# Performance work log

Measured on AMD Instinct MI355X. Metric: run time of the kernel, lower is better.

The kernel has to match this reference:

```python
import jax, jax.numpy as jnp
import numpy as np

B, T, C, H = 2, 2048, 2048, 16
HD = C // H  # 128
WINDOW = 2048


def setup_inputs() -> dict:
    key = jax.random.key(0)
    k0, k1, k2 = jax.random.split(key, 3)
    s = 0.02  # GPT-2 style init scale
    return {
        "x": jax.random.normal(k0, (B, T, C), jnp.float32),
        "w_attn": jax.random.normal(k1, (3 * C, C), jnp.float32) * s,
        "b_attn": jnp.zeros((3 * C,), jnp.float32),
        "w_proj": jax.random.normal(k2, (C, C), jnp.float32) * s,
        "b_proj": jnp.zeros((C,), jnp.float32),
    }


def reference(x, w_attn, b_attn, w_proj, b_proj):
    Bb, Tt, Cc = x.shape
    # fused qkv projection (torch Linear: y = x @ W^T + b)
    qkv = x @ w_attn.T + b_attn                       # [B, T, 3C]
    q, k, v = jnp.split(qkv, 3, axis=2)

    def to_heads(t):
        return t.reshape(Bb, Tt, H, HD).transpose(0, 2, 1, 3)  # [B, H, T, HD]

    q, k, v = to_heads(q), to_heads(k), to_heads(v)
    K = k.shape[2]  # kv length (== T, no past_kv)

    attn = jnp.einsum('bhqd,bhkd->bhqk', q, k) / jnp.sqrt(jnp.float32(HD))
    # Faithful to source: mask[:, :, T-1:T, :K] — single tril row T-1 broadcast
    # over all query positions (for prefill K==T this row is all ones).
    mask_row = jnp.arange(K) <= (Tt - 1)              # [K] bool
    attn = jnp.where(mask_row[None, None, None, :], attn, -jnp.inf)
    weights = jax.nn.softmax(attn, axis=-1)            # [B, H, T, K]
    # dropout p=0.0 (eval): identity
    ctx = jnp.einsum('bhqk,bhkd->bhqd', weights, v)    # [B, H, T, HD]
    ctx = ctx.transpose(0, 2, 1, 3).reshape(Bb, Tt, Cc)
    out = ctx @ w_proj.T + b_proj                      # [B, T, C]
    return (out, k, v)  # (context, present_kv)
```

## Files before the change

### kernel.cpp

```cpp
#include <hip/hip_runtime.h>
#include <hip/hip_bf16.h>
#include <cstdint>
#include <cstddef>
#include <cmath>

typedef __attribute__((ext_vector_type(8))) short short8;
typedef __attribute__((ext_vector_type(4))) short bf16x4;
typedef __attribute__((ext_vector_type(4))) float f32x4;

static constexpr int BB = 2, T = 2048, C = 2048, H = 16, HD = 128;
static constexpr int M = BB * T;
static constexpr size_t BTC = (size_t)BB * T * C;

__device__ __forceinline__ short f2bf(float f) {
    union { float f; uint32_t u; } v; v.f = f;
    uint32_t u = v.u;
    uint32_t r = (u + 0x7fffu + ((u >> 16) & 1u)) >> 16;
    return (short)r;
}

__device__ __forceinline__ short f2bf_fast(float f) {
    __hip_bfloat16 h = __float2bfloat16(f);
    return *reinterpret_cast<short*>(&h);
}

__device__ __forceinline__ void gl_lds16(const void* g, void* l) {
    __builtin_amdgcn_global_load_lds(
        (const __attribute__((address_space(1))) unsigned int*)g,
        (__attribute__((address_space(3))) unsigned int*)l, 16, 0, 0);
}

__global__ void cvt_bf16(const float* __restrict__ in, short* __restrict__ out, int n) {
    int i = (blockIdx.x * 256 + threadIdx.x) * 8;
    if (i >= n) return;
    float4 a = *(const float4*)(in + i);
    float4 b = *(const float4*)(in + i + 4);
    short8 o;
    o[0] = f2bf(a.x); o[1] = f2bf(a.y); o[2] = f2bf(a.z); o[3] = f2bf(a.w);
    o[4] = f2bf(b.x); o[5] = f2bf(b.y); o[6] = f2bf(b.z); o[7] = f2bf(b.w);
    *(short8*)(out + i) = o;
}

template<int NI, int EPI, int NBX>
__launch_bounds__(512, 2)
__global__ void gemm8p(const short* __restrict__ A, const short* __restrict__ Bw,
                       const float* __restrict__ bias, float* __restrict__ outF,
                       short* __restrict__ q_ws, short* __restrict__ k_ws, int Ndim) {
    extern __shared__ char lds[];
    constexpr int K = 2048, NKT = K / 64;
    constexpr int NCH = 4 + NI;
    constexpr int BUFSZ = 32768 + NI * 8192;

    int bid = blockIdx.x;
    int nwg = gridDim.x;
    int swz = (bid & 7) * (nwg >> 3) + (bid >> 3);
    int by = swz / NBX, bx = swz % NBX;
    int row0 = by * 256, col0 = bx * (NI * 64);

    int t = threadIdx.x, w = t >> 6, l = t & 63;
    int lr = l & 15, lg = l >> 4;
    int wr = w >> 2, wc = w & 3;

    const char* srcb[NCH];
    int dstoff[NCH];
#pragma unroll
    for (int c = 0; c < NCH; c++) {
        bool isA = c < 4;
        int coff = (isA ? c : c - 4) * 8192 + t * 16;
        int row = coff >> 7;
        int colb = (coff & 127) ^ ((row & 7) << 4);
        srcb[c] = isA ? (const char*)A + (size_t)(row0 + row) * (K * 2) + colb
                      : (const char*)Bw + (size_t)(col0 + row) * (K * 2) + colb;
        dstoff[c] = (isA ? 0 : 32768) + coff;
    }

    f32x4 acc[8][NI] = {};

#pragma unroll
    for (int c = 0; c < NCH; c++) gl_lds16(srcb[c], lds + dstoff[c]);
#pragma unroll
    for (int c = 0; c < NCH; c++) gl_lds16(srcb[c] + 128, lds + BUFSZ + dstoff[c]);
    asm volatile("s_waitcnt vmcnt(%0)" :: "n"(NCH) : "memory");
    __builtin_amdgcn_s_barrier();

    for (int kt = 0; kt < NKT; kt++) {
        char* base = lds + (kt & 1) * BUFSZ;
        const char* Bbase = base + 32768;
        int koff = (kt + 2) * 128;
        bool pf = (kt + 2 < NKT);

        short8 bfr[NI][2];
#pragma unroll
        for (int p = 0; p < 4; p++) {
            short8 af[2][2];
#pragma unroll
            for (int mi2 = 0; mi2 < 2; mi2++) {
                int row = wr * 128 + p * 32 + mi2 * 16 + lr;
#pragma unroll
                for (int ks = 0; ks < 2; ks++)
                    af[mi2][ks] = *(const short8*)(base + row * 128 +
                                  ((ks * 64 + lg * 16) ^ ((row & 7) << 4)));
            }
            if (p == 0) {
#pragma unroll
                for (int ni = 0; ni < NI; ni++) {
                    int row = wc * (NI * 16) + ni * 16 + lr;
#pragma unroll
                    for (int ks = 0; ks < 2; ks++)
                        bfr[ni][ks] = *(const short8*)(Bbase + row * 128 +
                                      ((ks * 64 + lg * 16) ^ ((row & 7) << 4)));
                }
            }
            __builtin_amdgcn_s_barrier();
            __builtin_amdgcn_s_setprio(1);
#pragma unroll
            for (int ks = 0; ks < 2; ks++)
#pragma unroll
                for (int mi2 = 0; mi2 < 2; mi2++)
#pragma unroll
                    for (int ni = 0; ni < NI; ni++)
                        acc[p * 2 + mi2][ni] = __builtin_amdgcn_mfma_f32_16x16x32_bf16(
                            af[mi2][ks], bfr[ni][ks], acc[p * 2 + mi2][ni], 0, 0, 0);
            __builtin_amdgcn_s_setprio(0);
            __builtin_amdgcn_sched_barrier(0);
            __builtin_amdgcn_s_barrier();

            if (p == 0 && pf) {
                asm volatile("" ::: "memory");
#pragma unroll
                for (int c = 4; c < NCH; c++) gl_lds16(srcb[c] + koff, base + dstoff[c]);
            }
            if (p == 1 && pf) {
                asm volatile("" ::: "memory");
                gl_lds16(srcb[0] + koff, base + dstoff[0]);
                gl_lds16(srcb[2] + koff, base + dstoff[2]);
            }
            if (p == 3) {
                if (pf) {
                    asm volatile("" ::: "memory");
                    gl_lds16(srcb[1] + koff, base + dstoff[1]);
                    gl_lds16(srcb[3] + koff, base + dstoff[3]);
                    asm volatile("s_waitcnt vmcnt(%0)" :: "n"(NCH) : "memory");
                } else {
                    asm volatile("s_waitcnt vmcnt(0)" ::: "memory");
                }
                __builtin_amdgcn_s_barrier();
            }
        }
    }

#pragma unroll
    for (int mi = 0; mi < 8; mi++) {
        int gr0 = row0 + wr * 128 + mi * 16 + lg * 4;
#pragma unroll
        for (int ni = 0; ni < NI; ni++) {
            int gc = col0 + wc * (NI * 16) + ni * 16 + lr;
            float bv = bias[gc];
            if (EPI == 0) {
                int sec = gc >> 11, cc = gc & 2047;
                int h = cc >> 7, d = cc & 127;
#pragma unroll
                for (int r = 0; r < 4; r++) {
                    float val = acc[mi][ni][r] + bv;
                    int gr = gr0 + r;
                    int b = gr >> 11, tt = gr & 2047;
                    size_t idx = ((size_t)(b * H + h) * T + tt) * HD + d;
                    if (sec == 0) {
                        q_ws[idx] = f2bf(val);
                    } else if (sec == 1) {
                        outF[BTC + idx] = val;
                        k_ws[idx] = f2bf(val);
                    } else {
                        outF[2 * BTC + idx] = val;
                    }
                }
            } else {
#pragma unroll
                for (int r = 0; r < 4; r++)
                    outF[(size_t)(gr0 + r) * Ndim + gc] = acc[mi][ni][r] + bv;
            }
        }
    }
}

__global__ void vtrans(const float* __restrict__ vin, short* __restrict__ vT) {
    __shared__ float tile[64 * 65];
    int blk = blockIdx.x;
    int bh = blk >> 6, rem = blk & 63;
    int t0 = (rem >> 1) * 64, d0 = (rem & 1) * 64;
    const float* src = vin + (size_t)bh * T * HD;
    short* dst = vT + (size_t)bh * HD * T;
    int t = threadIdx.x;
#pragma unroll
    for (int i = 0; i < 16; i++) {
        int idx = i * 256 + t;
        int r = idx >> 6, c = idx & 63;
        tile[r * 65 + c] = src[(size_t)(t0 + r) * HD + d0 + c];
    }
    __syncthreads();
#pragma unroll
    for (int i = 0; i < 16; i++) {
        int idx = i * 256 + t;
        int rd = idx >> 6, cc = idx & 63;
        dst[(size_t)(d0 + rd) * T + t0 + cc] = f2bf(tile[cc * 65 + rd]);
    }
}

__launch_bounds__(256, 2)
__global__ void attn_fwd(const short* __restrict__ q_ws, const short* __restrict__ k_ws,
                         const short* __restrict__ vT_ws, short* __restrict__ ctx) {
    __shared__ __attribute__((aligned(16))) char K_lds[2][64 * 256];
    __shared__ __attribute__((aligned(16))) char VT_lds[2][128 * 128];
    __shared__ __attribute__((aligned(16))) char P_lds[4][16 * 128];

    int bid = blockIdx.x;
    int blk = (bid & 7) * 64 + (bid >> 3);
    int bh = blk >> 4;
    int q0 = (blk & 15) * 128;
    int b = bh >> 4, h = bh & 15;
    int t = threadIdx.x, w = t >> 6, l = t & 63;
    int lr = l & 15, lg = l >> 4;
    int sw = (lr & 7) << 4;

    short8 qf[2][4];
#pragma unroll
    for (int qt = 0; qt < 2; qt++) {
        const short* Qp = q_ws + ((size_t)bh * T + q0 + w * 32 + qt * 16 + lr) * HD;
#pragma unroll
        for (int c = 0; c < 4; c++) qf[qt][c] = *(const short8*)(Qp + c * 32 + lg * 8);
    }

    const char* Kp = (const char*)(k_ws + (size_t)bh * T * HD);
    const short* VTp = vT_ws + (size_t)bh * HD * T;
    char* Pc = P_lds[w];

    const float SC = 0.12753123813884803f;
    float m[2] = {-INFINITY, -INFINITY}, lsum[2] = {0.f, 0.f};
    f32x4 acc[2][8] = {};

    auto STAGE = [&](int kt, int bsel) {
#pragma unroll
        for (int i = 0; i < 4; i++) {
            int off = i * 4096 + t * 16;
            int swzK = off ^ (((off >> 8) & 7) << 4);
            gl_lds16(Kp + (size_t)kt * 16384 + swzK, K_lds[bsel] + off);
            int swzV = off ^ (((off >> 7) & 7) << 4);
            int row = swzV >> 7, cole = (swzV & 127) >> 1;
            gl_lds16(VTp + (size_t)row * T + kt * 64 + cole, VT_lds[bsel] + off);
        }
    };

    STAGE(0, 0);
    asm volatile("s_waitcnt vmcnt(0)" ::: "memory");
    __syncthreads();

    for (int kt = 0; kt < T / 64; kt++) {
        int cur = kt & 1;
        if (kt + 1 < T / 64) STAGE(kt + 1, cur ^ 1);
        const char* Kc = K_lds[cur];
        const char* Vc = VT_lds[cur];

        f32x4 sacc[2][4] = {};
#pragma unroll
        for (int kj = 0; kj < 4; kj++) {
            int rowb = (kj * 16 + lr) * 256;
#pragma unroll
            for (int c = 0; c < 4; c++) {
                short8 kf = *(const short8*)(Kc + ((rowb + c * 64 + lg * 16) ^ sw));
                sacc[0][kj] = __builtin_amdgcn_mfma_f32_16x16x32_bf16(kf, qf[0][c], sacc[0][kj], 0, 0, 0);
                sacc[1][kj] = __builtin_amdgcn_mfma_f32_16x16x32_bf16(kf, qf[1][c], sacc[1][kj], 0, 0, 0);
            }
        }

#pragma unroll
        for (int qt = 0; qt < 2; qt++) {
            float t0 = fmaxf(fmaxf(sacc[qt][0][0], sacc[qt][0][1]), fmaxf(sacc[qt][0][2], sacc[qt][0][3]));
            float t1 = fmaxf(fmaxf(sacc[qt][1][0], sacc[qt][1][1]), fmaxf(sacc[qt][1][2], sacc[qt][1][3]));
            float t2 = fmaxf(fmaxf(sacc[qt][2][0], sacc[qt][2][1]), fmaxf(sacc[qt][2][2], sacc[qt][2][3]));
            float t3 = fmaxf(fmaxf(sacc[qt][3][0], sacc[qt][3][1]), fmaxf(sacc[qt][3][2], sacc[qt][3][3]));
            float xm = fmaxf(fmaxf(t0, t1), fmaxf(t2, t3)) * SC;
            xm = fmaxf(xm, __shfl_xor(xm, 16));
            xm = fmaxf(xm, __shfl_xor(xm, 32));

            if (!__all(xm <= m[qt] + 8.0f)) {
                float mn = fmaxf(m[qt], xm);
                float al = __builtin_exp2f(m[qt] - mn);
                m[qt] = mn;
                lsum[qt] *= al;
                float ar[4];
#pragma unroll
                for (int r = 0; r < 4; r++) ar[r] = __shfl(al, lg * 4 + r);
#pragma unroll
                for (int nj = 0; nj < 8; nj++)
#pragma unroll
                    for (int r = 0; r < 4; r++) acc[qt][nj][r] *= ar[r];
            }

            float s0 = 0.f;
#pragma unroll
            for (int kj = 0; kj < 4; kj++) {
                bf16x4 pk;
#pragma unroll
                for (int r = 0; r < 4; r++) {
                    float pv = __builtin_exp2f(__builtin_fmaf(sacc[qt][kj][r], SC, -m[qt]));
                    s0 += pv;
                    pk[r] = f2bf_fast(pv);
                }
                *(bf16x4*)(Pc + ((lr * 128 + kj * 32 + lg * 8) ^ sw)) = pk;
            }
            s0 += __shfl_xor(s0, 16);
            s0 += __shfl_xor(s0, 32);
            lsum[qt] += s0;

            asm volatile("s_waitcnt lgkmcnt(0)" ::: "memory");

#pragma unroll
            for (int c2 = 0; c2 < 2; c2++) {
                short8 pf = *(const short8*)(Pc + ((lr * 128 + c2 * 64 + lg * 16) ^ sw));
#pragma unroll
                for (int nj = 0; nj < 8; nj++) {
                    short8 vf = *(const short8*)(Vc + (((nj * 16 + lr) * 128 + c2 * 64 + lg * 16) ^ sw));
                    acc[qt][nj] = __builtin_amdgcn_mfma_f32_16x16x32_bf16(pf, vf, acc[qt][nj], 0, 0, 0);
                }
            }
        }

        asm volatile("s_waitcnt vmcnt(0)" ::: "memory");
        __syncthreads();
    }

#pragma unroll
    for (int qt = 0; qt < 2; qt++)
#pragma unroll
        for (int r = 0; r < 4; r++) {
            float rs = __shfl(lsum[qt], lg * 4 + r);
            float inv = 1.0f / rs;
            int tq = q0 + w * 32 + qt * 16 + lg * 4 + r;
            size_t base = ((size_t)b * T + tq) * C + h * HD;
#pragma unroll
            for (int nj = 0; nj < 8; nj++)
                ctx[base + nj * 16 + lr] = f2bf_fast(acc[qt][nj][r] * inv);
        }
}

extern "C" void kernel_launch(void* const* d_in, const int* in_sizes, int n_in,
                              void* d_out, int out_size, void* d_ws, size_t ws_size,
                              hipStream_t stream) {
    const float* x      = (const float*)d_in[0];
    const float* w_attn = (const float*)d_in[1];
    const float* b_attn = (const float*)d_in[2];
    const float* w_proj = (const float*)d_in[3];
    const float* b_proj = (const float*)d_in[4];
    float* out = (float*)d_out;

    char* ws = (char*)d_ws;
    short* x_bf  = (short*)ws;
    short* wp_bf = (short*)ws;
    short* wa_bf = (short*)(ws + 16777216);
    short* ctx   = (short*)(ws + 16777216);
    short* vT    = (short*)(ws + 41943040);

    short* q_ws = (short*)d_out;
    short* k_ws = (short*)d_out + BTC;

    hipFuncSetAttribute((const void*)gemm8p<3, 0, 32>,
                        hipFuncAttributeMaxDynamicSharedMemorySize, 114688);
    hipFuncSetAttribute((const void*)gemm8p<2, 1, 16>,
                        hipFuncAttributeMaxDynamicSharedMemorySize, 98304);

    cvt_bf16<<<4096, 256, 0, stream>>>(x, x_bf, (int)BTC);
    cvt_bf16<<<6144, 256, 0, stream>>>(w_attn, wa_bf, 3 * C * C);

    gemm8p<3, 0, 32><<<512, 512, 114688, stream>>>(x_bf, wa_bf, b_attn, out, q_ws, k_ws, 6144);

    vtrans<<<2048, 256, 0, stream>>>(out + 2 * BTC, vT);
    cvt_bf16<<<2048, 256, 0, stream>>>(w_proj, wp_bf, C * C);

    attn_fwd<<<512, 256, 0, stream>>>(q_ws, k_ws, vT, ctx);

    gemm8p<2, 1, 16><<<256, 512, 98304, stream>>>(ctx, wp_bf, b_proj, out, nullptr, nullptr, 2048);
}
```

Before: 293.7 us.

## Replace QKV GEMM with smaller-tile kernel and fuse V transpose into epilogue

```diff
diff --git a/kernel.cpp b/kernel.cpp
--- a/kernel.cpp
+++ b/kernel.cpp
@@ -41,11 +41,122 @@
     *(short8*)(out + i) = o;
 }
 
+__launch_bounds__(512, 4)
+__global__ void gemm_qkv128(const short* __restrict__ A, const short* __restrict__ Bw,
+                            const float* __restrict__ bias, float* __restrict__ outF,
+                            short* __restrict__ q_ws, short* __restrict__ k_ws,
+                            short* __restrict__ vT) {
+    extern __shared__ char lds[];
+    constexpr int K = 2048, NKT = K / 64;
+    constexpr int BUFSZ = 40960;
+
+    int bid = blockIdx.x;
+    int swz = (bid & 7) * 128 + (bid >> 3);
+    int by = swz >> 5, bx = swz & 31;
+    int row0 = by * 128, col0 = bx * 192;
+
+    int t = threadIdx.x, w = t >> 6, l = t & 63;
+    int lr = l & 15, lg = l >> 4;
+    int wr = w >> 2, wc = w & 3;
+
+    const char* srcb[5];
+    int dstoff[5];
+#pragma unroll
+    for (int c = 0; c < 5; c++) {
+        bool isA = c < 2;
+        int coff = (isA ? c : c - 2) * 8192 + t * 16;
+        int row = coff >> 7;
+        int colb = (coff & 127) ^ ((row & 7) << 4);
+        srcb[c] = isA ? (const char*)A + (size_t)(row0 + row) * (K * 2) + colb
+                      : (const char*)Bw + (size_t)(col0 + row) * (K * 2) + colb;
+        dstoff[c] = (isA ? 0 : 16384) + coff;
+    }
+
+    f32x4 acc[4][3] = {};
+
+#pragma unroll
+    for (int c = 0; c < 5; c++) gl_lds16(srcb[c], lds + dstoff[c]);
+#pragma unroll
+    for (int c = 0; c < 5; c++) gl_lds16(srcb[c] + 128, lds + BUFSZ + dstoff[c]);
+    asm volatile("s_waitcnt vmcnt(5)" ::: "memory");
+    __builtin_amdgcn_s_barrier();
+
+    for (int kt = 0; kt < NKT; kt++) {
+        char* base = lds + (kt & 1) * BUFSZ;
+        const char* Bbase = base + 16384;
+
+        short8 bfr[3][2];
+#pragma unroll
+        for (int ni = 0; ni < 3; ni++) {
+            int row = wc * 48 + ni * 16 + lr;
+            int rsw = (row & 7) << 4;
+#pragma unroll
+            for (int ks = 0; ks < 2; ks++)
+                bfr[ni][ks] = *(const short8*)(Bbase + row * 128 + ((ks * 64 + lg * 16) ^ rsw));
+        }
+        __builtin_amdgcn_s_setprio(1);
+#pragma unroll
+        for (int mi = 0; mi < 4; mi++) {
+            int row = wr * 64 + mi * 16 + lr;
+            int rsw = (row & 7) << 4;
+            const char* rp = base + row * 128;
+            short8 a0 = *(const short8*)(rp + ((lg * 16) ^ rsw));
+            short8 a1 = *(const short8*)(rp + ((64 + lg * 16) ^ rsw));
+#pragma unroll
+            for (int ni = 0; ni < 3; ni++) {
+                acc[mi][ni] = __builtin_amdgcn_mfma_f32_16x16x32_bf16(a0, bfr[ni][0], acc[mi][ni], 0, 0, 0);
+                acc[mi][ni] = __builtin_amdgcn_mfma_f32_16x16x32_bf16(a1, bfr[ni][1], acc[mi][ni], 0, 0, 0);
+            }
+        }
+        __builtin_amdgcn_s_setprio(0);
+
+        __builtin_amdgcn_s_barrier();
+        if (kt + 2 < NKT) {
+            int koff = (kt + 2) * 128;
+#pragma unroll
+            for (int c = 0; c < 5; c++) gl_lds16(srcb[c] + koff, base + dstoff[c]);
+            asm volatile("s_waitcnt vmcnt(5)" ::: "memory");
+        } else {
+            asm volatile("s_waitcnt vmcnt(0)" ::: "memory");
+        }
+        __builtin_amdgcn_s_barrier();
+    }
+
+#pragma unroll
+    for (int mi = 0; mi < 4; mi++) {
+        int gr0 = row0 + wr * 64 + mi * 16 + lg * 4;
+#pragma unroll
+        for (int ni = 0; ni < 3; ni++) {
+            int gc = col0 + wc * 48 + ni * 16 + lr;
+            float bv = bias[gc];
+            int sec = gc >> 11, cc = gc & 2047;
+            int h = cc >> 7, d = cc & 127;
+#pragma unroll
+            for (int r = 0; r < 4; r++) {
+                float val = acc[mi][ni][r] + bv;
+                int gr = gr0 + r;
+                int b = gr >> 11, tt = gr & 2047;
+                int bh = b * H + h;
+                size_t idx = ((size_t)bh * T + tt) * HD + d;
+                if (sec == 0) {
+                    q_ws[idx] = f2bf(val);
+                } else if (sec == 1) {
+                    outF[BTC + idx] = val;
+                    k_ws[idx] = f2bf(val);
+                } else {
+                    outF[2 * BTC + idx] = val;
+                    vT[((size_t)bh * HD + d) * T + tt] = f2bf(val);
+                }
+            }
+        }
+    }
+}
+
 template<int NI, int EPI, int NBX>
 __launch_bounds__(512, 2)
 __global__ void gemm8p(const short* __restrict__ A, const short* __restrict__ Bw,
                        const float* __restrict__ bias, float* __restrict__ outF,
-                       short* __restrict__ q_ws, short* __restrict__ k_ws, int Ndim) {
+                       int Ndim) {
     extern __shared__ char lds[];
     constexpr int K = 2048, NKT = K / 64;
     constexpr int NCH = 4 + NI;
@@ -122,22 +233,18 @@
                         acc[p * 2 + mi2][ni] = __builtin_amdgcn_mfma_f32_16x16x32_bf16(
                             af[mi2][ks], bfr[ni][ks], acc[p * 2 + mi2][ni], 0, 0, 0);
             __builtin_amdgcn_s_setprio(0);
-            __builtin_amdgcn_sched_barrier(0);
             __builtin_amdgcn_s_barrier();
 
             if (p == 0 && pf) {
-                asm volatile("" ::: "memory");
 #pragma unroll
                 for (int c = 4; c < NCH; c++) gl_lds16(srcb[c] + koff, base + dstoff[c]);
             }
             if (p == 1 && pf) {
-                asm volatile("" ::: "memory");
                 gl_lds16(srcb[0] + koff, base + dstoff[0]);
                 gl_lds16(srcb[2] + koff, base + dstoff[2]);
             }
             if (p == 3) {
                 if (pf) {
-                    asm volatile("" ::: "memory");
                     gl_lds16(srcb[1] + koff, base + dstoff[1]);
                     gl_lds16(srcb[3] + koff, base + dstoff[3]);
                     asm volatile("s_waitcnt vmcnt(%0)" :: "n"(NCH) : "memory");
@@ -156,53 +263,10 @@
         for (int ni = 0; ni < NI; ni++) {
             int gc = col0 + wc * (NI * 16) + ni * 16 + lr;
             float bv = bias[gc];
-            if (EPI == 0) {
-                int sec = gc >> 11, cc = gc & 2047;
-                int h = cc >> 7, d = cc & 127;
-#pragma unroll
-                for (int r = 0; r < 4; r++) {
-                    float val = acc[mi][ni][r] + bv;
-                    int gr = gr0 + r;
-                    int b = gr >> 11, tt = gr & 2047;
-                    size_t idx = ((size_t)(b * H + h) * T + tt) * HD + d;
-                    if (sec == 0) {
-                        q_ws[idx] = f2bf(val);
-                    } else if (sec == 1) {
-                        outF[BTC + idx] = val;
-                        k_ws[idx] = f2bf(val);
-                    } else {
-                        outF[2 * BTC + idx] = val;
-                    }
-                }
-            } else {
-#pragma unroll
-                for (int r = 0; r < 4; r++)
-                    outF[(size_t)(gr0 + r) * Ndim + gc] = acc[mi][ni][r] + bv;
-            }
-        }
-    }
-}
-
-__global__ void vtrans(const float* __restrict__ vin, short* __restrict__ vT) {
-    __shared__ float tile[64 * 65];
-    int blk = blockIdx.x;
-    int bh = blk >> 6, rem = blk & 63;
-    int t0 = (rem >> 1) * 64, d0 = (rem & 1) * 64;
-    const float* src = vin + (size_t)bh * T * HD;
-    short* dst = vT + (size_t)bh * HD * T;
-    int t = threadIdx.x;
-#pragma unroll
-    for (int i = 0; i < 16; i++) {
-        int idx = i * 256 + t;
-        int r = idx >> 6, c = idx & 63;
-        tile[r * 65 + c] = src[(size_t)(t0 + r) * HD + d0 + c];
-    }
-    __syncthreads();
-#pragma unroll
-    for (int i = 0; i < 16; i++) {
-        int idx = i * 256 + t;
-        int rd = idx >> 6, cc = idx & 63;
-        dst[(size_t)(d0 + rd) * T + t0 + cc] = f2bf(tile[cc * 65 + rd]);
+#pragma unroll
+            for (int r = 0; r < 4; r++)
+                outF[(size_t)(gr0 + r) * Ndim + gc] = acc[mi][ni][r] + bv;
+        }
     }
 }
 
@@ -316,11 +380,11 @@
 
 #pragma unroll
             for (int c2 = 0; c2 < 2; c2++) {
-                short8 pf = *(const short8*)(Pc + ((lr * 128 + c2 * 64 + lg * 16) ^ sw));
+                short8 pf2 = *(const short8*)(Pc + ((lr * 128 + c2 * 64 + lg * 16) ^ sw));
 #pragma unroll
                 for (int nj = 0; nj < 8; nj++) {
                     short8 vf = *(const short8*)(Vc + (((nj * 16 + lr) * 128 + c2 * 64 + lg * 16) ^ sw));
-                    acc[qt][nj] = __builtin_amdgcn_mfma_f32_16x16x32_bf16(pf, vf, acc[qt][nj], 0, 0, 0);
+                    acc[qt][nj] = __builtin_amdgcn_mfma_f32_16x16x32_bf16(pf2, vf, acc[qt][nj], 0, 0, 0);
                 }
             }
         }
@@ -363,20 +427,19 @@
     short* q_ws = (short*)d_out;
     short* k_ws = (short*)d_out + BTC;
 
-    hipFuncSetAttribute((const void*)gemm8p<3, 0, 32>,
-                        hipFuncAttributeMaxDynamicSharedMemorySize, 114688);
+    hipFuncSetAttribute((const void*)gemm_qkv128,
+                        hipFuncAttributeMaxDynamicSharedMemorySize, 81920);
     hipFuncSetAttribute((const void*)gemm8p<2, 1, 16>,
                         hipFuncAttributeMaxDynamicSharedMemorySize, 98304);
 
     cvt_bf16<<<4096, 256, 0, stream>>>(x, x_bf, (int)BTC);
     cvt_bf16<<<6144, 256, 0, stream>>>(w_attn, wa_bf, 3 * C * C);
 
-    gemm8p<3, 0, 32><<<512, 512, 114688, stream>>>(x_bf, wa_bf, b_attn, out, q_ws, k_ws, 6144);
-
-    vtrans<<<2048, 256, 0, stream>>>(out + 2 * BTC, vT);
+    gemm_qkv128<<<1024, 512, 81920, stream>>>(x_bf, wa_bf, b_attn, out, q_ws, k_ws, vT);
+
     cvt_bf16<<<2048, 256, 0, stream>>>(w_proj, wp_bf, C * C);
 
     attn_fwd<<<512, 256, 0, stream>>>(q_ws, k_ws, vT, ctx);
 
-    gemm8p<2, 1, 16><<<256, 512, 98304, stream>>>(ctx, wp_bf, b_proj, out, nullptr, nullptr, 2048);
-}
+    gemm8p<2, 1, 16><<<256, 512, 98304, stream>>>(ctx, wp_bf, b_proj, out, 2048);
+}
```

After: 349.1 us. +18.9%, slower.
